# Optimization experiments

Measured on AMD Instinct MI355X. Metric: run time of the kernel, lower is better.

The kernel has to match this reference:

```python
import jax, jax.numpy as jnp
import numpy as np

B, T, D_OBS = 64, 512, 128
D_LAT, D_HID, K = 16, 256, 8
VAR = 0.0005
LOG2PI = float(np.log(2.0 * np.pi))


def _leaky(x):
    return jnp.where(x > 0, x, 0.01 * x)


def setup_inputs() -> dict:
    key = jax.random.key(0)
    ks = jax.random.split(key, 12)
    s = 0.05
    return {
        "x": jax.random.normal(ks[0], (B, T, D_OBS), jnp.float32),
        "eps": jax.random.normal(ks[1], (B, T, D_LAT), jnp.float32),
        "W1": jax.random.normal(ks[2], (D_OBS, D_HID), jnp.float32) * s,
        "b1": jnp.zeros((D_HID,), jnp.float32),
        "W2": jax.random.normal(ks[3], (D_HID, 2 * D_LAT), jnp.float32) * s,
        "b2": jnp.zeros((2 * D_LAT,), jnp.float32),
        "Wt1": jax.random.normal(ks[4], (K, D_LAT, D_HID), jnp.float32) * s,
        "bt1": jnp.zeros((K, D_HID), jnp.float32),
        "Wt2": jax.random.normal(ks[5], (K, D_HID, D_LAT), jnp.float32) * s,
        "bt2": jnp.zeros((K, D_LAT), jnp.float32),
        "Wd1": jax.random.normal(ks[6], (D_LAT, D_HID), jnp.float32) * s,
        "bd1": jnp.zeros((D_HID,), jnp.float32),
        "Wd2": jax.random.normal(ks[7], (D_HID, D_OBS), jnp.float32) * s,
        "bd2": jnp.zeros((D_OBS,), jnp.float32),
        "Q": jax.random.normal(ks[8], (K, K), jnp.float32) * 0.1,
        "pi": jax.random.normal(ks[9], (K,), jnp.float32) * 0.1,
        "init_mean": jax.random.normal(ks[10], (K, D_LAT), jnp.float32),
        "init_cov": jax.random.uniform(ks[11], (K, 1, 1), jnp.float32) * jnp.eye(D_LAT, dtype=jnp.float32)[None] * 5.0,
        "covs": jnp.tile(jnp.eye(D_LAT, dtype=jnp.float32)[None], (K, 1, 1)),
    }


def _mvn_logprob(diff, chol):
    # diff [..., K, d]; chol [K, d, d] lower Cholesky of per-state covariance
    d = chol.shape[-1]
    Linv = jax.scipy.linalg.solve_triangular(
        chol, jnp.broadcast_to(jnp.eye(d, dtype=chol.dtype), chol.shape), lower=True)
    sol = jnp.einsum('kij,...kj->...ki', Linv, diff)
    logdet = 2.0 * jnp.sum(jnp.log(jnp.diagonal(chol, axis1=-2, axis2=-1)), -1)  # [K]
    return -0.5 * (d * LOG2PI + logdet + jnp.sum(sol * sol, -1))


def _forward(x, eps, W1, b1, W2, b2, Wt1, bt1, Wt2, bt2, Wd1, bd1, Wd2, bd2,
             Q, pi, init_mean, init_cov, covs):
    Bx = x.shape[0]
    dz = init_mean.shape[-1]
    # ---- factored MLP encoder: x -> (mu, logvar); reparameterized sample ----
    h = _leaky(x @ W1 + b1)
    enc = h @ W2 + b2
    z_mu, z_log_var = enc[..., :dz], enc[..., dz:]
    z = z_mu + jnp.exp(0.5 * z_log_var) * eps                            # [B,T,dz]
    # ---- local evidence log p(z_t | z_{t-1}, s_t=k) ----
    jitter = 1e-6 * jnp.eye(dz, dtype=x.dtype)
    L0 = jnp.linalg.cholesky(init_cov @ jnp.swapaxes(init_cov, -1, -2) + jitter)
    ev1 = _mvn_logprob(z[:, 0:1, None, :] - init_mean[None, None], L0)   # [B,1,K]
    ht = jax.nn.softplus(jnp.einsum('btd,kdh->btkh', z[:, :-1], Wt1) + bt1)
    means = jnp.einsum('btkh,khd->btkd', ht, Wt2) + bt2                  # [B,T-1,K,dz]
    Lt = jnp.linalg.cholesky(covs @ jnp.swapaxes(covs, -1, -2) + jitter)
    evT = _mvn_logprob(z[:, 1:, None, :] - means, Lt)                    # [B,T-1,K]
    ev = jnp.concatenate([ev1, evT], axis=1)                             # [B,T,K]
    # ---- HMM alpha recursion in log domain (temperature=1) ----
    log_pi = jax.nn.log_softmax(pi)
    Qlog = jax.nn.log_softmax(Q, axis=-1).T                              # [new, old]
    lp0 = ev[:, 0] + log_pi
    lZ0 = jax.scipy.special.logsumexp(lp0, axis=-1)
    la0 = lp0 - lZ0[:, None]

    def step(la, ev_t):
        lp = jax.scipy.special.logsumexp(ev_t[:, :, None] + Qlog[None] + la[:, None, :], axis=-1)
        lZ = jax.scipy.special.logsumexp(lp, axis=-1)
        return lp - lZ[:, None], lZ

    _, lZs = jax.lax.scan(step, la0, jnp.moveaxis(ev[:, 1:], 1, 0))
    log_Z = lZ0 + jnp.sum(lZs, axis=0)                                   # [B]
    # ---- decoder ----
    x_hat = _leaky(z @ Wd1 + bd1) @ Wd2 + bd2
    # ---- ELBO ----
    recon = jnp.sum(-0.5 * jnp.log(2.0 * jnp.pi * VAR) - (x - x_hat) ** 2 / (2.0 * VAR)) / Bx
    logq = -0.5 * (dz * LOG2PI + jnp.sum(z_log_var, -1)
                   + jnp.sum((z - z_mu) ** 2 / jnp.exp(z_log_var), -1))
    entropy_q = -jnp.sum(logq) / Bx
    msm = jnp.sum(log_Z) / Bx
    loss = -(recon + entropy_q + msm)
    return x_hat, z, loss


def reference(x, eps, W1, b1, W2, b2, Wt1, bt1, Wt2, bt2, Wd1, bd1, Wd2, bd2,
              Q, pi, init_mean, init_cov, covs):
    return _forward(x, eps, W1, b1, W2, b2, Wt1, bt1, Wt2, bt2, Wd1, bd1, Wd2, bd2,
                    Q, pi, init_mean, init_cov, covs)
```

## Files before the change

### kernel.cpp

```cpp
#include <hip/hip_runtime.h>
#include <math.h>

#define B_SZ   64
#define T_SZ   512
#define DOBS   128
#define DLAT   16
#define DHID   256
#define K_SZ   8
#define ROWS_T 32704
#define ROWS_A 32768

#define LOG2PI_F 1.8378770664093453f
#define VAR_F    5.0e-4f

#define LINV0_OFF   16
#define LOGDET0_OFF 2064
#define LINVT_OFF   2080
#define LOGDETT_OFF 4128

#define Z_OUT_OFF   4194304
#define LOSS_OFF    4718592
#define PBUF_OFF  262144
#define ACC_OFF   327680

typedef __attribute__((ext_vector_type(8))) short short8;
typedef __attribute__((ext_vector_type(4))) float floatx4;

__device__ __forceinline__ float leakyf(float v) { return v > 0.f ? v : 0.01f * v; }
__device__ __forceinline__ unsigned short f2bf(float f) {
  union { float f; unsigned int u; } v; v.f = f;
  unsigned int lsb = (v.u >> 16) & 1;
  v.u += 0x7fffu + lsb;
  return (unsigned short)(v.u >> 16);
}

__global__ __launch_bounds__(256) void prep_kernel(const float* __restrict__ init_cov,
                                                   const float* __restrict__ covs,
                                                   float* __restrict__ ws) {
  __shared__ float M[16][16];
  __shared__ float L[16][16];
  __shared__ float X[16][17];
  int job = blockIdx.x;
  const float* C = (job < 8) ? (init_cov + job * 256) : (covs + (job - 8) * 256);
  float* linv = ws + ((job < 8) ? (LINV0_OFF + job * 256) : (LINVT_OFF + (job - 8) * 256));
  float* logdet = ws + ((job < 8) ? (LOGDET0_OFF + job) : (LOGDETT_OFF + (job - 8)));
  int tid = threadIdx.x;
  int i = tid >> 4, j = tid & 15;
  {
    float s = (i == j) ? 1e-6f : 0.f;
    #pragma unroll
    for (int p = 0; p < 16; ++p) s += C[i * 16 + p] * C[j * 16 + p];
    M[i][j] = s;
  }
  __syncthreads();
  for (int c = 0; c < 16; ++c) {
    if (tid == 0) {
      float s = M[c][c];
      for (int p = 0; p < c; ++p) s -= L[c][p] * L[c][p];
      L[c][c] = sqrtf(s);
    }
    __syncthreads();
    if (tid > c && tid < 16) {
      float s = M[tid][c];
      for (int p = 0; p < c; ++p) s -= L[tid][p] * L[c][p];
      L[tid][c] = s / L[c][c];
    }
    __syncthreads();
  }
  if (tid < 16) {
    for (int r = 0; r < 16; ++r) {
      float s = (r == tid) ? 1.f : 0.f;
      for (int p = tid; p < r; ++p) s -= L[r][p] * X[p][tid];
      X[r][tid] = (r >= tid) ? s / L[r][r] : 0.f;
    }
  }
  __syncthreads();
  linv[i * 16 + j] = X[i][j];
  if (tid == 0) {
    float s = 0.f;
    for (int d = 0; d < 16; ++d) s += logf(L[d][d]);
    *logdet = 2.f * s;
  }
}

__global__ __launch_bounds__(256) void enc_kernel(
    const float* __restrict__ x, const float* __restrict__ eps,
    const float* __restrict__ W1, const float* __restrict__ b1,
    const float* __restrict__ W2, const float* __restrict__ b2,
    float* __restrict__ z_out, float* __restrict__ ws) {
  __shared__ __align__(16) unsigned short w1t[256 * 136];
  __shared__ __align__(16) unsigned short w2t[32 * 264];
  __shared__ __align__(16) unsigned short hbuf[4 * 16 * 264];
  __shared__ float sred;
  int tid = threadIdx.x;
  if (tid == 0) sred = 0.f;
  for (int e = tid; e < 32768; e += 256) {
    int k = e >> 8, n = e & 255;
    w1t[n * 136 + k] = f2bf(W1[e]);
  }
  for (int e = tid; e < 8192; e += 256) {
    int k = e >> 5, n = e & 31;
    w2t[n * 264 + k] = f2bf(W2[e]);
  }
  __syncthreads();

  int wid = tid >> 6, lane = tid & 63;
  int m = lane & 15, quad = lane >> 4;
  unsigned short* hb = hbuf + wid * (16 * 264);
  float logq_acc = 0.f;

  #pragma unroll
  for (int tile = 0; tile < 2; ++tile) {
    long rowb = (long)blockIdx.x * 128 + wid * 32 + tile * 16;
    short8 xa[4];
    const float* xp = x + (rowb + m) * 128 + quad * 8;
    #pragma unroll
    for (int kt = 0; kt < 4; ++kt) {
      float4 f0 = *(const float4*)(xp + kt * 32);
      float4 f1 = *(const float4*)(xp + kt * 32 + 4);
      short8 v;
      v[0] = (short)f2bf(f0.x); v[1] = (short)f2bf(f0.y);
      v[2] = (short)f2bf(f0.z); v[3] = (short)f2bf(f0.w);
      v[4] = (short)f2bf(f1.x); v[5] = (short)f2bf(f1.y);
      v[6] = (short)f2bf(f1.z); v[7] = (short)f2bf(f1.w);
      xa[kt] = v;
    }
    #pragma unroll 4
    for (int c = 0; c < 16; ++c) {
      float bias = b1[c * 16 + m];
      floatx4 a1 = {bias, bias, bias, bias};
      #pragma unroll
      for (int kt = 0; kt < 4; ++kt) {
        short8 bf = *(const short8*)&w1t[(c * 16 + m) * 136 + kt * 32 + quad * 8];
        a1 = __builtin_amdgcn_mfma_f32_16x16x32_bf16(xa[kt], bf, a1, 0, 0, 0);
      }
      #pragma unroll
      for (int g = 0; g < 4; ++g)
        hb[(quad * 4 + g) * 264 + c * 16 + m] = f2bf(leakyf(a1[g]));
    }
    float bm0 = b2[m], bm1 = b2[16 + m];
    floatx4 a20 = {bm0, bm0, bm0, bm0};
    floatx4 a21 = {bm1, bm1, bm1, bm1};
    #pragma unroll
    for (int kt = 0; kt < 8; ++kt) {
      short8 ha = *(const short8*)&hb[m * 264 + kt * 32 + quad * 8];
      short8 wb0 = *(const short8*)&w2t[m * 264 + kt * 32 + quad * 8];
      short8 wb1 = *(const short8*)&w2t[(16 + m) * 264 + kt * 32 + quad * 8];
      a20 = __builtin_amdgcn_mfma_f32_16x16x32_bf16(ha, wb0, a20, 0, 0, 0);
      a21 = __builtin_amdgcn_mfma_f32_16x16x32_bf16(ha, wb1, a21, 0, 0, 0);
    }
    #pragma unroll
    for (int g = 0; g < 4; ++g) {
      long row = rowb + quad * 4 + g;
      float mu = a20[g], lv = a21[g];
      float ev = eps[row * 16 + m];
      float zv = mu + __expf(0.5f * lv) * ev;
      z_out[row * 16 + m] = zv;
      float zz = zv - mu;
      logq_acc += lv + zz * zz * __expf(-lv);
    }
  }
  #pragma unroll
  for (int off = 1; off < 64; off <<= 1) logq_acc += __shfl_xor(logq_acc, off, 64);
  if (lane == 0) atomicAdd(&sred, -0.5f * logq_acc);
  __syncthreads();
  if (tid == 0) atomicAdd(&ws[1], sred - 0.5f * 16.f * LOG2PI_F * 128.f);
}

__global__ __launch_bounds__(256) void ev0_kernel(const float* __restrict__ z,
                                                  const float* __restrict__ init_mean,
                                                  const float* __restrict__ ws,
                                                  float* __restrict__ evT) {
  int gid = blockIdx.x * 256 + threadIdx.x;
  if (gid >= B_SZ * K_SZ) return;
  int k = gid & 7, b = gid >> 3;
  const float* zr = z + (long)b * T_SZ * 16;
  const float* linv = ws + LINV0_OFF + k * 256;
  float diff[16];
  #pragma unroll
  for (int d = 0; d < 16; ++d) diff[d] = zr[d] - init_mean[k * 16 + d];
  float quad = 0.f;
  #pragma unroll
  for (int i2 = 0; i2 < 16; ++i2) {
    float s = 0.f;
    #pragma unroll
    for (int jj = 0; jj < 16; ++jj) s += linv[i2 * 16 + jj] * diff[jj];
    quad += s * s;
  }
  evT[(long)b * 4096 + (long)k * 512] =
      -0.5f * (16.f * LOG2PI_F + ws[LOGDET0_OFF + k] + quad);
}

__global__ __launch_bounds__(256) void evt_kernel(
    const float* __restrict__ z, const float* __restrict__ Wt1,
    const float* __restrict__ bt1, const float* __restrict__ Wt2,
    const float* __restrict__ bt2, const float* __restrict__ ws,
    float* __restrict__ evT) {
  __shared__ __align__(16) unsigned short w1t[256 * 24];
  __shared__ __align__(16) unsigned short w2t[16 * 264];
  __shared__ __align__(16) unsigned short hbuf[4 * 16 * 264];
  __shared__ __align__(16) unsigned short dbuf[4 * 16 * 24];
  __shared__ __align__(16) unsigned short linvb[16 * 24];
  int tid = threadIdx.x;
  int k = blockIdx.y;
  const float* w1g = Wt1 + k * 4096;
  const float* w2g = Wt2 + k * 4096;
  #pragma unroll
  for (int it = 0; it < 16; ++it)
    w1t[tid * 24 + it] = f2bf(w1g[it * 256 + tid]);
  #pragma unroll
  for (int it = 0; it < 16; ++it) {
    int e = tid + it * 256;
    w2t[(e & 15) * 264 + (e >> 4)] = f2bf(w2g[e]);
  }
  { int i = tid >> 4, j = tid & 15;
    linvb[i * 24 + j] = f2bf(ws[LINVT_OFF + k * 256 + tid]); }
  float logdetk = ws[LOGDETT_OFF + k];
  __syncthreads();

  int wid = tid >> 6;
  int lane = tid & 63;
  int m = lane & 15, quad = lane >> 4;
  long wave_base = (long)blockIdx.x * 64 + wid * 16;
  unsigned short* hb = hbuf + wid * (16 * 264);
  unsigned short* db = dbuf + wid * (16 * 24);

  short8 za = (short8)0;
  if (quad < 2) {
    const float* zp = z + (wave_base + m) * 16 + quad * 8;
    float4 f0 = *(const float4*)zp;
    float4 f1 = *(const float4*)(zp + 4);
    za[0] = (short)f2bf(f0.x); za[1] = (short)f2bf(f0.y);
    za[2] = (short)f2bf(f0.z); za[3] = (short)f2bf(f0.w);
    za[4] = (short)f2bf(f1.x); za[5] = (short)f2bf(f1.y);
    za[6] = (short)f2bf(f1.z); za[7] = (short)f2bf(f1.w);
  }

  const float* bt1g = bt1 + k * 256;
  #pragma unroll 4
  for (int c = 0; c < 16; ++c) {
    short8 bfrag = (short8)0;
    if (quad < 2) bfrag = *(const short8*)&w1t[(c * 16 + m) * 24 + quad * 8];
    float bias = bt1g[c * 16 + m];
    floatx4 a1 = {bias, bias, bias, bias};
    a1 = __builtin_amdgcn_mfma_f32_16x16x32_bf16(za, bfrag, a1, 0, 0, 0);
    #pragma unroll
    for (int g = 0; g < 4; ++g) {
      float v = a1[g];
      float t = __expf(-fabsf(v));
      float sp = fmaxf(v, 0.f) + __logf(1.f + t);
      hb[(quad * 4 + g) * 264 + c * 16 + m] = f2bf(sp);
    }
  }

  float btv = bt2[k * 16 + m];
  floatx4 a2 = {btv, btv, btv, btv};
  #pragma unroll
  for (int kt = 0; kt < 8; ++kt) {
    short8 ha = *(const short8*)&hb[m * 264 + kt * 32 + quad * 8];
    short8 wb = *(const short8*)&w2t[m * 264 + kt * 32 + quad * 8];
    a2 = __builtin_amdgcn_mfma_f32_16x16x32_bf16(ha, wb, a2, 0, 0, 0);
  }

  #pragma unroll
  for (int g = 0; g < 4; ++g) {
    long grow = wave_base + quad * 4 + g;
    float znx = (grow + 1 < ROWS_A) ? z[(grow + 1) * 16 + m] : 0.f;
    db[(quad * 4 + g) * 24 + m] = f2bf(znx - a2[g]);
  }
  short8 da = (short8)0, lb = (short8)0;
  if (quad < 2) {
    da = *(const short8*)&db[m * 24 + quad * 8];
    lb = *(const short8*)&linvb[m * 24 + quad * 8];
  }
  floatx4 a3 = {0.f, 0.f, 0.f, 0.f};
  a3 = __builtin_amdgcn_mfma_f32_16x16x32_bf16(da, lb, a3, 0, 0, 0);
  #pragma unroll
  for (int g = 0; g < 4; ++g) {
    float v = a3[g];
    v = v * v;
    v += __shfl_xor(v, 1, 64);
    v += __shfl_xor(v, 2, 64);
    v += __shfl_xor(v, 4, 64);
    v += __shfl_xor(v, 8, 64);
    long grow = wave_base + quad * 4 + g;
    if (m == 0 && (grow & 511) != 511) {
      long r1 = grow + 1;
      evT[(r1 >> 9) * 4096 + (long)k * 512 + (r1 & 511)] =
          -0.5f * (16.f * LOG2PI_F + logdetk + v);
    }
  }
}

__global__ __launch_bounds__(256) void hmm_scan(const float* __restrict__ Q,
                                                const float* __restrict__ evT,
                                                float* __restrict__ pbuf,
                                                float* __restrict__ accbuf) {
  int tid = threadIdx.x;
  int wid = tid >> 6, lane = tid & 63;
  int job = blockIdx.x * 4 + wid;
  int b = job >> 4, c = job & 15;
  int i = lane >> 3, j = lane & 7;

  float qp[8];
  #pragma unroll
  for (int p = 0; p < 8; ++p) {
    float mr = Q[p * 8 + 0];
    #pragma unroll
    for (int cc = 1; cc < 8; ++cc) mr = fmaxf(mr, Q[p * 8 + cc]);
    float rs = 0.f;
    #pragma unroll
    for (int cc = 0; cc < 8; ++cc) rs += __expf(Q[p * 8 + cc] - mr);
    qp[p] = __expf(Q[p * 8 + i] - mr) / rs;
  }
  float qself;
  {
    float mr = Q[j * 8 + 0];
    #pragma unroll
    for (int cc = 1; cc < 8; ++cc) mr = fmaxf(mr, Q[j * 8 + cc]);
    float rs = 0.f;
    #pragma unroll
    for (int cc = 0; cc < 8; ++cc) rs += __expf(Q[j * 8 + cc] - mr);
    qself = __expf(Q[j * 8 + i] - mr) / rs;
  }

  int t0 = 1 + c * 32;
  int L = (c == 15) ? 31 : 32;
  const float* evI = evT + (long)b * 4096 + (long)i * 512 + t0;

  float f[32];
  float accm = 0.f;
  #pragma unroll
  for (int s = 0; s < 32; ++s) {
    float e = (s < L) ? evI[s] : 0.f;
    float m = e;
    m = fmaxf(m, __shfl_xor(m, 8, 64));
    m = fmaxf(m, __shfl_xor(m, 16, 64));
    m = fmaxf(m, __shfl_xor(m, 32, 64));
    f[s] = __expf(e - m);
    if (s < L) accm += m;
  }

  float P = f[0] * qself;
  #pragma unroll
  for (int s = 1; s < 32; ++s) {
    if (s < L) {
      float a0 = __shfl(P, j,      64);
      float a1 = __shfl(P, 8 + j,  64);
      float a2 = __shfl(P, 16 + j, 64);
      float a3 = __shfl(P, 24 + j, 64);
      float a4 = __shfl(P, 32 + j, 64);
      float a5 = __shfl(P, 40 + j, 64);
      float a6 = __shfl(P, 48 + j, 64);
      float a7 = __shfl(P, 56 + j, 64);
      float sv = ((qp[0] * a0 + qp[1] * a1) + (qp[2] * a2 + qp[3] * a3))
               + ((qp[4] * a4 + qp[5] * a5) + (qp[6] * a6 + qp[7] * a7));
      P = f[s] * sv;
    }
    if ((s & 7) == 7) {
      float mx = P;
      mx = fmaxf(mx, __shfl_xor(mx, 1, 64));
      mx = fmaxf(mx, __shfl_xor(mx, 2, 64));
      mx = fmaxf(mx, __shfl_xor(mx, 4, 64));
      mx = fmaxf(mx, __shfl_xor(mx, 8, 64));
      mx = fmaxf(mx, __shfl_xor(mx, 16, 64));
      mx = fmaxf(mx, __shfl_xor(mx, 32, 64));
      mx = fmaxf(mx, 1e-30f);
      P = P / mx;
      accm += __logf(mx);
    }
  }
  pbuf[(long)job * 64 + lane] = P;
  if (lane == 0) accbuf[job] = accm;
}

__global__ __launch_bounds__(512) void hmm_comb(const float* __restrict__ pi,
                                                const float* __restrict__ evT,
                                                const float* __restrict__ pbuf,
                                                const float* __restrict__ accbuf,
                                                float* __restrict__ ws) {
  int tid = threadIdx.x;
  int wid = tid >> 6, lane = tid & 63;
  int b = blockIdx.x * 8 + wid;
  int j = lane & 7;

  float mp = pi[0];
  #pragma unroll
  for (int cc = 1; cc < 8; ++cc) mp = fmaxf(mp, pi[cc]);
  float sp = 0.f;
  #pragma unroll
  for (int cc = 0; cc < 8; ++cc) sp += __expf(pi[cc] - mp);
  float lpi = pi[j] - mp - __logf(sp);

  float lp0 = evT[(long)b * 4096 + (long)j * 512] + lpi;
  float m0 = lp0;
  m0 = fmaxf(m0, __shfl_xor(m0, 1, 64));
  m0 = fmaxf(m0, __shfl_xor(m0, 2, 64));
  m0 = fmaxf(m0, __shfl_xor(m0, 4, 64));
  float u = __expf(lp0 - m0);
  double acc = (double)m0;

  #pragma unroll
  for (int c = 0; c < 16; ++c) {
    float P = pbuf[((long)b * 16 + c) * 64 + lane];
    float contrib = P * u;
    contrib += __shfl_xor(contrib, 1, 64);
    contrib += __shfl_xor(contrib, 2, 64);
    contrib += __shfl_xor(contrib, 4, 64);
    u = __shfl(contrib, j * 9, 64);
    float mxu = u;
    mxu = fmaxf(mxu, __shfl_xor(mxu, 1, 64));
    mxu = fmaxf(mxu, __shfl_xor(mxu, 2, 64));
    mxu = fmaxf(mxu, __shfl_xor(mxu, 4, 64));
    mxu = fmaxf(mxu, 1e-30f);
    u = u / mxu;
    acc += (double)(__logf(mxu) + accbuf[b * 16 + c]);
  }
  float su = u;
  su += __shfl_xor(su, 1, 64);
  su += __shfl_xor(su, 2, 64);
  su += __shfl_xor(su, 4, 64);
  float logZ = (float)(acc + (double)__logf(su));
  if (lane == 0) atomicAdd(&ws[2], logZ);
}

__global__ __launch_bounds__(256) void dec_kernel(
    const float* __restrict__ x, const float* __restrict__ z,
    const float* __restrict__ Wd1, const float* __restrict__ bd1,
    const float* __restrict__ Wd2, const float* __restrict__ bd2,
    float* __restrict__ xhat, float* __restrict__ ws) {
  __shared__ __align__(16) unsigned short w1t[256 * 24];
  __shared__ __align__(16) unsigned short w2t[128 * 264];
  __shared__ __align__(16) unsigned short hbuf[4 * 16 * 264];
  __shared__ float sred;
  int tid = threadIdx.x;
  if (tid == 0) sred = 0.f;
  for (int e = tid; e < 4096; e += 256) {
    int k = e >> 8, n = e & 255;
    w1t[n * 24 + k] = f2bf(Wd1[e]);
  }
  for (int e = tid; e < 32768; e += 256) {
    int k = e >> 7, n = e & 127;
    w2t[n * 264 + k] = f2bf(Wd2[e]);
  }
  __syncthreads();

  int wid = tid >> 6, lane = tid & 63;
  int m = lane & 15, quad = lane >> 4;
  unsigned short* hb = hbuf + wid * (16 * 264);
  const float C0 = -0.5f * logf(6.2831853071795864f * VAR_F);
  float rsum = 0.f;

  #pragma unroll
  for (int tile = 0; tile < 2; ++tile) {
    long rowb = (long)blockIdx.x * 128 + wid * 32 + tile * 16;
    short8 za = (short8)0;
    if (quad < 2) {
      const float* zp = z + (rowb + m) * 16 + quad * 8;
      float4 f0 = *(const float4*)zp;
      float4 f1 = *(const float4*)(zp + 4);
      za[0] = (short)f2bf(f0.x); za[1] = (short)f2bf(f0.y);
      za[2] = (short)f2bf(f0.z); za[3] = (short)f2bf(f0.w);
      za[4] = (short)f2bf(f1.x); za[5] = (short)f2bf(f1.y);
      za[6] = (short)f2bf(f1.z); za[7] = (short)f2bf(f1.w);
    }
    #pragma unroll 4
    for (int c = 0; c < 16; ++c) {
      short8 bfrag = (short8)0;
      if (quad < 2) bfrag = *(const short8*)&w1t[(c * 16 + m) * 24 + quad * 8];
      float bias = bd1[c * 16 + m];
      floatx4 a1 = {bias, bias, bias, bias};
      a1 = __builtin_amdgcn_mfma_f32_16x16x32_bf16(za, bfrag, a1, 0, 0, 0);
      #pragma unroll
      for (int g = 0; g < 4; ++g)
        hb[(quad * 4 + g) * 264 + c * 16 + m] = f2bf(leakyf(a1[g]));
    }
    floatx4 a2[8];
    #pragma unroll
    for (int c2 = 0; c2 < 8; ++c2) {
      float bv = bd2[c2 * 16 + m];
      a2[c2] = (floatx4){bv, bv, bv, bv};
    }
    #pragma unroll
    for (int kt = 0; kt < 8; ++kt) {
      short8 ha = *(const short8*)&hb[m * 264 + kt * 32 + quad * 8];
      #pragma unroll
      for (int c2 = 0; c2 < 8; ++c2) {
        short8 wb = *(const short8*)&w2t[(c2 * 16 + m) * 264 + kt * 32 + quad * 8];
        a2[c2] = __builtin_amdgcn_mfma_f32_16x16x32_bf16(ha, wb, a2[c2], 0, 0, 0);
      }
    }
    #pragma unroll
    for (int c2 = 0; c2 < 8; ++c2) {
      int col = c2 * 16 + m;
      #pragma unroll
      for (int g = 0; g < 4; ++g) {
        long row = rowb + quad * 4 + g;
        float xh = a2[c2][g];
        xhat[row * 128 + col] = xh;
        float dd = x[row * 128 + col] - xh;
        rsum += C0 - dd * dd * (0.5f / VAR_F);
      }
    }
  }
  #pragma unroll
  for (int off = 1; off < 64; off <<= 1) rsum += __shfl_xor(rsum, off, 64);
  if (lane == 0) atomicAdd(&sred, rsum);
  __syncthreads();
  if (tid == 0) atomicAdd(&ws[0], sred);
}

__global__ void fin_kernel(const float* __restrict__ ws, float* __restrict__ out) {
  float loss = -((ws[0] - ws[1] + ws[2]) * (1.f / 64.f));
  out[LOSS_OFF] = loss;
}

extern "C" void kernel_launch(void* const* d_in, const int* in_sizes, int n_in,
                              void* d_out, int out_size, void* d_ws, size_t ws_size,
                              hipStream_t stream) {
  (void)in_sizes; (void)n_in; (void)out_size; (void)ws_size;
  const float* x   = (const float*)d_in[0];
  const float* eps = (const float*)d_in[1];
  const float* W1  = (const float*)d_in[2];
  const float* b1  = (const float*)d_in[3];
  const float* W2  = (const float*)d_in[4];
  const float* b2  = (const float*)d_in[5];
  const float* Wt1 = (const float*)d_in[6];
  const float* bt1 = (const float*)d_in[7];
  const float* Wt2 = (const float*)d_in[8];
  const float* bt2 = (const float*)d_in[9];
  const float* Wd1 = (const float*)d_in[10];
  const float* bd1 = (const float*)d_in[11];
  const float* Wd2 = (const float*)d_in[12];
  const float* bd2 = (const float*)d_in[13];
  const float* Q   = (const float*)d_in[14];
  const float* pi  = (const float*)d_in[15];
  const float* im  = (const float*)d_in[16];
  const float* ic  = (const float*)d_in[17];
  const float* cv  = (const float*)d_in[18];
  float* out = (float*)d_out;
  float* ws  = (float*)d_ws;
  float* z_out = out + Z_OUT_OFF;
  float* evT  = out;
  float* pbuf = out + PBUF_OFF;
  float* accb = out + ACC_OFF;

  hipMemsetAsync(ws, 0, 16, stream);
  prep_kernel<<<16, 256, 0, stream>>>(ic, cv, ws);
  enc_kernel<<<256, 256, 0, stream>>>(x, eps, W1, b1, W2, b2, z_out, ws);
  ev0_kernel<<<2, 256, 0, stream>>>(z_out, im, ws, evT);
  evt_kernel<<<dim3(512, 8), 256, 0, stream>>>(z_out, Wt1, bt1, Wt2, bt2, ws, evT);
  hmm_scan<<<256, 256, 0, stream>>>(Q, evT, pbuf, accb);
  hmm_comb<<<8, 512, 0, stream>>>(pi, evT, pbuf, accb, ws);
  dec_kernel<<<256, 256, 0, stream>>>(x, z_out, Wd1, bd1, Wd2, bd2, out, ws);
  fin_kernel<<<1, 1, 0, stream>>>(ws, out);
}
```

Measured before the change: 261.9 us.

## Preconvert weights to bf16 image once and restructure enc/evt/dec MLP kernels

Adds a single wcvt kernel that converts and transposes all weights into a padded bf16 image in workspace, so enc/evt/dec no longer re-convert weights per block. Enc and dec now read W1/Wd2 fragments straight from global memory and fuse the hidden-layer chunk into the second GEMM through a small per-wave tile, which cuts LDS use and lets the grid grow to 512 blocks. Evt handles four tiles per block with fewer blocks, folding the first-step emission into hmm_comb and removing ev0_kernel. The memset moves into prep_kernel. The catch is an extra launch plus global-memory weight fragment reads that may cost more than they save.

After: 252.2 us. 1.04x faster.

```diff
diff --git a/kernel.cpp b/kernel.cpp
--- a/kernel.cpp
+++ b/kernel.cpp
@@ -7,7 +7,6 @@
 #define DLAT   16
 #define DHID   256
 #define K_SZ   8
-#define ROWS_T 32704
 #define ROWS_A 32768
 
 #define LOG2PI_F 1.8378770664093453f
@@ -17,6 +16,16 @@
 #define LOGDET0_OFF 2064
 #define LINVT_OFF   2080
 #define LOGDETT_OFF 4128
+#define WIMG_F_OFF  8192
+
+#define EVT_W1   0
+#define EVT_W2   49152
+#define EVT_LINV 82944
+#define ENC_W1   86016
+#define ENC_W2   120832
+#define DEC_W1   129280
+#define DEC_W2   135424
+#define WCVT_TOTAL 141568
 
 #define Z_OUT_OFF   4194304
 #define LOSS_OFF    4718592
@@ -24,6 +33,7 @@
 #define ACC_OFF   327680
 
 typedef __attribute__((ext_vector_type(8))) short short8;
+typedef __attribute__((ext_vector_type(8))) unsigned short ush8;
 typedef __attribute__((ext_vector_type(4))) float floatx4;
 
 __device__ __forceinline__ float leakyf(float v) { return v > 0.f ? v : 0.01f * v; }
@@ -45,6 +55,7 @@
   float* linv = ws + ((job < 8) ? (LINV0_OFF + job * 256) : (LINVT_OFF + (job - 8) * 256));
   float* logdet = ws + ((job < 8) ? (LOGDET0_OFF + job) : (LOGDETT_OFF + (job - 8)));
   int tid = threadIdx.x;
+  if (job == 0 && tid < 4) ws[tid] = 0.f;
   int i = tid >> 4, j = tid & 15;
   {
     float s = (i == j) ? 1e-6f : 0.f;
@@ -83,211 +94,209 @@
   }
 }
 
+__global__ __launch_bounds__(256) void wcvt_kernel(
+    const float* __restrict__ Wt1, const float* __restrict__ Wt2,
+    const float* __restrict__ W1, const float* __restrict__ W2,
+    const float* __restrict__ Wd1, const float* __restrict__ Wd2,
+    const float* __restrict__ ws, unsigned short* __restrict__ wimg) {
+  for (int e = blockIdx.x * 256 + threadIdx.x; e < WCVT_TOTAL; e += gridDim.x * 256) {
+    if (e < 32768) {
+      int k = e >> 12, r = e & 4095, i = r >> 4, d = r & 15;
+      wimg[EVT_W1 + k * 6144 + i * 24 + d] = f2bf(Wt1[k * 4096 + d * 256 + i]);
+    } else if (e < 65536) {
+      int e2 = e - 32768; int k = e2 >> 12, r = e2 & 4095, h = r >> 4, d2 = r & 15;
+      wimg[EVT_W2 + k * 4224 + d2 * 264 + h] = f2bf(Wt2[k * 4096 + h * 16 + d2]);
+    } else if (e < 67584) {
+      int e2 = e - 65536; int k = e2 >> 8, r = e2 & 255, i = r >> 4, j = r & 15;
+      wimg[EVT_LINV + k * 384 + i * 24 + j] = f2bf(ws[LINVT_OFF + k * 256 + i * 16 + j]);
+    } else if (e < 100352) {
+      int e2 = e - 67584; int n = e2 >> 7, kk = e2 & 127;
+      wimg[ENC_W1 + n * 136 + kk] = f2bf(W1[kk * 256 + n]);
+    } else if (e < 108544) {
+      int e2 = e - 100352; int n = e2 >> 8, kk = e2 & 255;
+      wimg[ENC_W2 + n * 264 + kk] = f2bf(W2[kk * 32 + n]);
+    } else if (e < 112640) {
+      int e2 = e - 108544; int n = e2 >> 4, kk = e2 & 15;
+      wimg[DEC_W1 + n * 24 + kk] = f2bf(Wd1[kk * 256 + n]);
+    } else {
+      int e2 = e - 112640; int n = e2 & 127, kk = e2 >> 7;
+      wimg[DEC_W2 + n * 264 + kk] = f2bf(Wd2[kk * 128 + n]);
+    }
+  }
+}
+
 __global__ __launch_bounds__(256) void enc_kernel(
     const float* __restrict__ x, const float* __restrict__ eps,
-    const float* __restrict__ W1, const float* __restrict__ b1,
-    const float* __restrict__ W2, const float* __restrict__ b2,
+    const float* __restrict__ b1, const float* __restrict__ b2,
+    const unsigned short* __restrict__ wimg,
     float* __restrict__ z_out, float* __restrict__ ws) {
-  __shared__ __align__(16) unsigned short w1t[256 * 136];
   __shared__ __align__(16) unsigned short w2t[32 * 264];
-  __shared__ __align__(16) unsigned short hbuf[4 * 16 * 264];
+  __shared__ __align__(16) unsigned short ttile[4][16 * 56];
+  __shared__ float b1s[256];
   __shared__ float sred;
   int tid = threadIdx.x;
   if (tid == 0) sred = 0.f;
-  for (int e = tid; e < 32768; e += 256) {
-    int k = e >> 8, n = e & 255;
-    w1t[n * 136 + k] = f2bf(W1[e]);
-  }
-  for (int e = tid; e < 8192; e += 256) {
-    int k = e >> 5, n = e & 31;
-    w2t[n * 264 + k] = f2bf(W2[e]);
+  {
+    const ush8* s2 = (const ush8*)(wimg + ENC_W2);
+    for (int e = tid; e < 1056; e += 256) ((ush8*)w2t)[e] = s2[e];
+    b1s[tid] = b1[tid];
   }
   __syncthreads();
 
   int wid = tid >> 6, lane = tid & 63;
   int m = lane & 15, quad = lane >> 4;
-  unsigned short* hb = hbuf + wid * (16 * 264);
-  float logq_acc = 0.f;
-
-  #pragma unroll
-  for (int tile = 0; tile < 2; ++tile) {
-    long rowb = (long)blockIdx.x * 128 + wid * 32 + tile * 16;
-    short8 xa[4];
-    const float* xp = x + (rowb + m) * 128 + quad * 8;
-    #pragma unroll
-    for (int kt = 0; kt < 4; ++kt) {
-      float4 f0 = *(const float4*)(xp + kt * 32);
-      float4 f1 = *(const float4*)(xp + kt * 32 + 4);
-      short8 v;
-      v[0] = (short)f2bf(f0.x); v[1] = (short)f2bf(f0.y);
-      v[2] = (short)f2bf(f0.z); v[3] = (short)f2bf(f0.w);
-      v[4] = (short)f2bf(f1.x); v[5] = (short)f2bf(f1.y);
-      v[6] = (short)f2bf(f1.z); v[7] = (short)f2bf(f1.w);
-      xa[kt] = v;
-    }
-    #pragma unroll 4
-    for (int c = 0; c < 16; ++c) {
-      float bias = b1[c * 16 + m];
+  unsigned short* tt = ttile[wid];
+  const unsigned short* w1i = wimg + ENC_W1;
+  long rowb = (long)blockIdx.x * 64 + wid * 16;
+
+  short8 xa[4];
+  const float* xp = x + (rowb + m) * 128 + quad * 8;
+  #pragma unroll
+  for (int kt = 0; kt < 4; ++kt) {
+    float4 f0 = *(const float4*)(xp + kt * 32);
+    float4 f1 = *(const float4*)(xp + kt * 32 + 4);
+    short8 v;
+    v[0] = (short)f2bf(f0.x); v[1] = (short)f2bf(f0.y);
+    v[2] = (short)f2bf(f0.z); v[3] = (short)f2bf(f0.w);
+    v[4] = (short)f2bf(f1.x); v[5] = (short)f2bf(f1.y);
+    v[6] = (short)f2bf(f1.z); v[7] = (short)f2bf(f1.w);
+    xa[kt] = v;
+  }
+  float bm0 = b2[m], bm1 = b2[16 + m];
+  floatx4 a20 = {bm0, bm0, bm0, bm0};
+  floatx4 a21 = {bm1, bm1, bm1, bm1};
+  #pragma unroll
+  for (int cp = 0; cp < 8; ++cp) {
+    #pragma unroll
+    for (int h = 0; h < 2; ++h) {
+      int c = cp * 2 + h;
+      float bias = b1s[c * 16 + m];
       floatx4 a1 = {bias, bias, bias, bias};
       #pragma unroll
       for (int kt = 0; kt < 4; ++kt) {
-        short8 bf = *(const short8*)&w1t[(c * 16 + m) * 136 + kt * 32 + quad * 8];
+        short8 bf = *(const short8*)&w1i[(c * 16 + m) * 136 + kt * 32 + quad * 8];
         a1 = __builtin_amdgcn_mfma_f32_16x16x32_bf16(xa[kt], bf, a1, 0, 0, 0);
       }
       #pragma unroll
       for (int g = 0; g < 4; ++g)
-        hb[(quad * 4 + g) * 264 + c * 16 + m] = f2bf(leakyf(a1[g]));
-    }
-    float bm0 = b2[m], bm1 = b2[16 + m];
-    floatx4 a20 = {bm0, bm0, bm0, bm0};
-    floatx4 a21 = {bm1, bm1, bm1, bm1};
-    #pragma unroll
-    for (int kt = 0; kt < 8; ++kt) {
-      short8 ha = *(const short8*)&hb[m * 264 + kt * 32 + quad * 8];
-      short8 wb0 = *(const short8*)&w2t[m * 264 + kt * 32 + quad * 8];
-      short8 wb1 = *(const short8*)&w2t[(16 + m) * 264 + kt * 32 + quad * 8];
-      a20 = __builtin_amdgcn_mfma_f32_16x16x32_bf16(ha, wb0, a20, 0, 0, 0);
-      a21 = __builtin_amdgcn_mfma_f32_16x16x32_bf16(ha, wb1, a21, 0, 0, 0);
-    }
-    #pragma unroll
-    for (int g = 0; g < 4; ++g) {
-      long row = rowb + quad * 4 + g;
-      float mu = a20[g], lv = a21[g];
-      float ev = eps[row * 16 + m];
-      float zv = mu + __expf(0.5f * lv) * ev;
-      z_out[row * 16 + m] = zv;
-      float zz = zv - mu;
-      logq_acc += lv + zz * zz * __expf(-lv);
-    }
+        tt[(quad * 4 + g) * 56 + h * 16 + m] = f2bf(leakyf(a1[g]));
+    }
+    short8 ha = *(const short8*)&tt[m * 56 + quad * 8];
+    short8 wb0 = *(const short8*)&w2t[m * 264 + cp * 32 + quad * 8];
+    short8 wb1 = *(const short8*)&w2t[(16 + m) * 264 + cp * 32 + quad * 8];
+    a20 = __builtin_amdgcn_mfma_f32_16x16x32_bf16(ha, wb0, a20, 0, 0, 0);
+    a21 = __builtin_amdgcn_mfma_f32_16x16x32_bf16(ha, wb1, a21, 0, 0, 0);
+  }
+  float logq_acc = 0.f;
+  #pragma unroll
+  for (int g = 0; g < 4; ++g) {
+    long row = rowb + quad * 4 + g;
+    float mu = a20[g], lv = a21[g];
+    float ev = eps[row * 16 + m];
+    float zv = mu + __expf(0.5f * lv) * ev;
+    z_out[row * 16 + m] = zv;
+    float zz = zv - mu;
+    logq_acc += lv + zz * zz * __expf(-lv);
   }
   #pragma unroll
   for (int off = 1; off < 64; off <<= 1) logq_acc += __shfl_xor(logq_acc, off, 64);
   if (lane == 0) atomicAdd(&sred, -0.5f * logq_acc);
   __syncthreads();
-  if (tid == 0) atomicAdd(&ws[1], sred - 0.5f * 16.f * LOG2PI_F * 128.f);
-}
-
-__global__ __launch_bounds__(256) void ev0_kernel(const float* __restrict__ z,
-                                                  const float* __restrict__ init_mean,
-                                                  const float* __restrict__ ws,
-                                                  float* __restrict__ evT) {
-  int gid = blockIdx.x * 256 + threadIdx.x;
-  if (gid >= B_SZ * K_SZ) return;
-  int k = gid & 7, b = gid >> 3;
-  const float* zr = z + (long)b * T_SZ * 16;
-  const float* linv = ws + LINV0_OFF + k * 256;
-  float diff[16];
-  #pragma unroll
-  for (int d = 0; d < 16; ++d) diff[d] = zr[d] - init_mean[k * 16 + d];
-  float quad = 0.f;
-  #pragma unroll
-  for (int i2 = 0; i2 < 16; ++i2) {
-    float s = 0.f;
-    #pragma unroll
-    for (int jj = 0; jj < 16; ++jj) s += linv[i2 * 16 + jj] * diff[jj];
-    quad += s * s;
-  }
-  evT[(long)b * 4096 + (long)k * 512] =
-      -0.5f * (16.f * LOG2PI_F + ws[LOGDET0_OFF + k] + quad);
+  if (tid == 0) atomicAdd(&ws[1], sred - 0.5f * 16.f * LOG2PI_F * 64.f);
 }
 
 __global__ __launch_bounds__(256) void evt_kernel(
-    const float* __restrict__ z, const float* __restrict__ Wt1,
-    const float* __restrict__ bt1, const float* __restrict__ Wt2,
-    const float* __restrict__ bt2, const float* __restrict__ ws,
-    float* __restrict__ evT) {
-  __shared__ __align__(16) unsigned short w1t[256 * 24];
-  __shared__ __align__(16) unsigned short w2t[16 * 264];
-  __shared__ __align__(16) unsigned short hbuf[4 * 16 * 264];
-  __shared__ __align__(16) unsigned short dbuf[4 * 16 * 24];
-  __shared__ __align__(16) unsigned short linvb[16 * 24];
+    const float* __restrict__ z, const unsigned short* __restrict__ wimg,
+    const float* __restrict__ bt1, const float* __restrict__ bt2,
+    const float* __restrict__ ws, float* __restrict__ evT) {
+  __shared__ __align__(16) unsigned short w1t[6144];
+  __shared__ __align__(16) unsigned short w2t[4224];
+  __shared__ __align__(16) unsigned short linvb[384];
+  __shared__ __align__(16) unsigned short ttile[4][16 * 56];
+  __shared__ __align__(16) unsigned short dtile[4][16 * 24];
+  __shared__ float bt1s[256];
   int tid = threadIdx.x;
   int k = blockIdx.y;
-  const float* w1g = Wt1 + k * 4096;
-  const float* w2g = Wt2 + k * 4096;
-  #pragma unroll
-  for (int it = 0; it < 16; ++it)
-    w1t[tid * 24 + it] = f2bf(w1g[it * 256 + tid]);
-  #pragma unroll
-  for (int it = 0; it < 16; ++it) {
-    int e = tid + it * 256;
-    w2t[(e & 15) * 264 + (e >> 4)] = f2bf(w2g[e]);
-  }
-  { int i = tid >> 4, j = tid & 15;
-    linvb[i * 24 + j] = f2bf(ws[LINVT_OFF + k * 256 + tid]); }
+  {
+    const ush8* s1 = (const ush8*)(wimg + EVT_W1 + k * 6144);
+    for (int e = tid; e < 768; e += 256) ((ush8*)w1t)[e] = s1[e];
+    const ush8* s2 = (const ush8*)(wimg + EVT_W2 + k * 4224);
+    for (int e = tid; e < 528; e += 256) ((ush8*)w2t)[e] = s2[e];
+    if (tid < 48) ((ush8*)linvb)[tid] = ((const ush8*)(wimg + EVT_LINV + k * 384))[tid];
+    bt1s[tid] = bt1[k * 256 + tid];
+  }
   float logdetk = ws[LOGDETT_OFF + k];
   __syncthreads();
 
-  int wid = tid >> 6;
-  int lane = tid & 63;
+  int wid = tid >> 6, lane = tid & 63;
   int m = lane & 15, quad = lane >> 4;
-  long wave_base = (long)blockIdx.x * 64 + wid * 16;
-  unsigned short* hb = hbuf + wid * (16 * 264);
-  unsigned short* db = dbuf + wid * (16 * 24);
-
-  short8 za = (short8)0;
-  if (quad < 2) {
-    const float* zp = z + (wave_base + m) * 16 + quad * 8;
-    float4 f0 = *(const float4*)zp;
-    float4 f1 = *(const float4*)(zp + 4);
-    za[0] = (short)f2bf(f0.x); za[1] = (short)f2bf(f0.y);
-    za[2] = (short)f2bf(f0.z); za[3] = (short)f2bf(f0.w);
-    za[4] = (short)f2bf(f1.x); za[5] = (short)f2bf(f1.y);
-    za[6] = (short)f2bf(f1.z); za[7] = (short)f2bf(f1.w);
-  }
-
-  const float* bt1g = bt1 + k * 256;
-  #pragma unroll 4
-  for (int c = 0; c < 16; ++c) {
-    short8 bfrag = (short8)0;
-    if (quad < 2) bfrag = *(const short8*)&w1t[(c * 16 + m) * 24 + quad * 8];
-    float bias = bt1g[c * 16 + m];
-    floatx4 a1 = {bias, bias, bias, bias};
-    a1 = __builtin_amdgcn_mfma_f32_16x16x32_bf16(za, bfrag, a1, 0, 0, 0);
+  unsigned short* tt = ttile[wid];
+  unsigned short* db = dtile[wid];
+  float btv = bt2[k * 16 + m];
+
+  #pragma unroll
+  for (int tile = 0; tile < 4; ++tile) {
+    long rowb = (long)blockIdx.x * 256 + wid * 64 + tile * 16;
+    short8 za = (short8)0;
+    if (quad < 2) {
+      const float* zp = z + (rowb + m) * 16 + quad * 8;
+      float4 f0 = *(const float4*)zp;
+      float4 f1 = *(const float4*)(zp + 4);
+      za[0] = (short)f2bf(f0.x); za[1] = (short)f2bf(f0.y);
+      za[2] = (short)f2bf(f0.z); za[3] = (short)f2bf(f0.w);
+      za[4] = (short)f2bf(f1.x); za[5] = (short)f2bf(f1.y);
+      za[6] = (short)f2bf(f1.z); za[7] = (short)f2bf(f1.w);
+    }
+    floatx4 a2 = {btv, btv, btv, btv};
+    #pragma unroll
+    for (int cp = 0; cp < 8; ++cp) {
+      #pragma unroll
+      for (int h = 0; h < 2; ++h) {
+        int c = cp * 2 + h;
+        short8 bfrag = (short8)0;
+        if (quad < 2) bfrag = *(const short8*)&w1t[(c * 16 + m) * 24 + quad * 8];
+        float bias = bt1s[c * 16 + m];
+        floatx4 a1 = {bias, bias, bias, bias};
+        a1 = __builtin_amdgcn_mfma_f32_16x16x32_bf16(za, bfrag, a1, 0, 0, 0);
+        #pragma unroll
+        for (int g = 0; g < 4; ++g) {
+          float v = a1[g];
+          float t = __expf(-fabsf(v));
+          float sp = fmaxf(v, 0.f) + __logf(1.f + t);
+          tt[(quad * 4 + g) * 56 + h * 16 + m] = f2bf(sp);
+        }
+      }
+      short8 ha = *(const short8*)&tt[m * 56 + quad * 8];
+      short8 wb = *(const short8*)&w2t[m * 264 + cp * 32 + quad * 8];
+      a2 = __builtin_amdgcn_mfma_f32_16x16x32_bf16(ha, wb, a2, 0, 0, 0);
+    }
     #pragma unroll
     for (int g = 0; g < 4; ++g) {
-      float v = a1[g];
-      float t = __expf(-fabsf(v));
-      float sp = fmaxf(v, 0.f) + __logf(1.f + t);
-      hb[(quad * 4 + g) * 264 + c * 16 + m] = f2bf(sp);
-    }
-  }
-
-  float btv = bt2[k * 16 + m];
-  floatx4 a2 = {btv, btv, btv, btv};
-  #pragma unroll
-  for (int kt = 0; kt < 8; ++kt) {
-    short8 ha = *(const short8*)&hb[m * 264 + kt * 32 + quad * 8];
-    short8 wb = *(const short8*)&w2t[m * 264 + kt * 32 + quad * 8];
-    a2 = __builtin_amdgcn_mfma_f32_16x16x32_bf16(ha, wb, a2, 0, 0, 0);
-  }
-
-  #pragma unroll
-  for (int g = 0; g < 4; ++g) {
-    long grow = wave_base + quad * 4 + g;
-    float znx = (grow + 1 < ROWS_A) ? z[(grow + 1) * 16 + m] : 0.f;
-    db[(quad * 4 + g) * 24 + m] = f2bf(znx - a2[g]);
-  }
-  short8 da = (short8)0, lb = (short8)0;
-  if (quad < 2) {
-    da = *(const short8*)&db[m * 24 + quad * 8];
-    lb = *(const short8*)&linvb[m * 24 + quad * 8];
-  }
-  floatx4 a3 = {0.f, 0.f, 0.f, 0.f};
-  a3 = __builtin_amdgcn_mfma_f32_16x16x32_bf16(da, lb, a3, 0, 0, 0);
-  #pragma unroll
-  for (int g = 0; g < 4; ++g) {
-    float v = a3[g];
-    v = v * v;
-    v += __shfl_xor(v, 1, 64);
-    v += __shfl_xor(v, 2, 64);
-    v += __shfl_xor(v, 4, 64);
-    v += __shfl_xor(v, 8, 64);
-    long grow = wave_base + quad * 4 + g;
-    if (m == 0 && (grow & 511) != 511) {
-      long r1 = grow + 1;
-      evT[(r1 >> 9) * 4096 + (long)k * 512 + (r1 & 511)] =
-          -0.5f * (16.f * LOG2PI_F + logdetk + v);
+      long grow = rowb + quad * 4 + g;
+      float znx = (grow + 1 < ROWS_A) ? z[(grow + 1) * 16 + m] : 0.f;
+      db[(quad * 4 + g) * 24 + m] = f2bf(znx - a2[g]);
+    }
+    short8 da = (short8)0, lb = (short8)0;
+    if (quad < 2) {
+      da = *(const short8*)&db[m * 24 + quad * 8];
+      lb = *(const short8*)&linvb[m * 24 + quad * 8];
+    }
+    floatx4 a3 = {0.f, 0.f, 0.f, 0.f};
+    a3 = __builtin_amdgcn_mfma_f32_16x16x32_bf16(da, lb, a3, 0, 0, 0);
+    #pragma unroll
+    for (int g = 0; g < 4; ++g) {
+      float v = a3[g];
+      v = v * v;
+      v += __shfl_xor(v, 1, 64);
+      v += __shfl_xor(v, 2, 64);
+      v += __shfl_xor(v, 4, 64);
+      v += __shfl_xor(v, 8, 64);
+      long grow = rowb + quad * 4 + g;
+      if (m == 0 && (grow & 511) != 511) {
+        long r1 = grow + 1;
+        evT[(r1 >> 9) * 4096 + (long)k * 512 + (r1 & 511)] =
+            -0.5f * (16.f * LOG2PI_F + logdetk + v);
+      }
     }
   }
 }
@@ -375,7 +384,8 @@
 }
 
 __global__ __launch_bounds__(512) void hmm_comb(const float* __restrict__ pi,
-                                                const float* __restrict__ evT,
+                                                const float* __restrict__ z,
+                                                const float* __restrict__ init_mean,
                                                 const float* __restrict__ pbuf,
                                                 const float* __restrict__ accbuf,
                                                 float* __restrict__ ws) {
@@ -392,7 +402,22 @@
   for (int cc = 0; cc < 8; ++cc) sp += __expf(pi[cc] - mp);
   float lpi = pi[j] - mp - __logf(sp);
 
-  float lp0 = evT[(long)b * 4096 + (long)j * 512] + lpi;
+  const float* zr = z + (long)b * 8192;
+  const float* linv = ws + LINV0_OFF + j * 256;
+  float diff[16];
+  #pragma unroll
+  for (int d = 0; d < 16; ++d) diff[d] = zr[d] - init_mean[j * 16 + d];
+  float quad0 = 0.f;
+  #pragma unroll
+  for (int i2 = 0; i2 < 16; ++i2) {
+    float s = 0.f;
+    #pragma unroll
+    for (int jj = 0; jj < 16; ++jj) s += linv[i2 * 16 + jj] * diff[jj];
+    quad0 += s * s;
+  }
+  float ev0 = -0.5f * (16.f * LOG2PI_F + ws[LOGDET0_OFF + j] + quad0);
+
+  float lp0 = ev0 + lpi;
   float m0 = lp0;
   m0 = fmaxf(m0, __shfl_xor(m0, 1, 64));
   m0 = fmaxf(m0, __shfl_xor(m0, 2, 64));
@@ -426,81 +451,79 @@
 
 __global__ __launch_bounds__(256) void dec_kernel(
     const float* __restrict__ x, const float* __restrict__ z,
-    const float* __restrict__ Wd1, const float* __restrict__ bd1,
-    const float* __restrict__ Wd2, const float* __restrict__ bd2,
+    const float* __restrict__ bd1, const float* __restrict__ bd2,
+    const unsigned short* __restrict__ wimg,
     float* __restrict__ xhat, float* __restrict__ ws) {
-  __shared__ __align__(16) unsigned short w1t[256 * 24];
-  __shared__ __align__(16) unsigned short w2t[128 * 264];
-  __shared__ __align__(16) unsigned short hbuf[4 * 16 * 264];
+  __shared__ __align__(16) unsigned short w1t[6144];
+  __shared__ __align__(16) unsigned short ttile[4][16 * 56];
+  __shared__ float bd1s[256];
+  __shared__ float bd2s[128];
   __shared__ float sred;
   int tid = threadIdx.x;
   if (tid == 0) sred = 0.f;
-  for (int e = tid; e < 4096; e += 256) {
-    int k = e >> 8, n = e & 255;
-    w1t[n * 24 + k] = f2bf(Wd1[e]);
-  }
-  for (int e = tid; e < 32768; e += 256) {
-    int k = e >> 7, n = e & 127;
-    w2t[n * 264 + k] = f2bf(Wd2[e]);
+  {
+    const ush8* s1 = (const ush8*)(wimg + DEC_W1);
+    for (int e = tid; e < 768; e += 256) ((ush8*)w1t)[e] = s1[e];
+    bd1s[tid] = bd1[tid];
+    if (tid < 128) bd2s[tid] = bd2[tid];
   }
   __syncthreads();
 
   int wid = tid >> 6, lane = tid & 63;
   int m = lane & 15, quad = lane >> 4;
-  unsigned short* hb = hbuf + wid * (16 * 264);
-  const float C0 = -0.5f * logf(6.2831853071795864f * VAR_F);
-  float rsum = 0.f;
-
-  #pragma unroll
-  for (int tile = 0; tile < 2; ++tile) {
-    long rowb = (long)blockIdx.x * 128 + wid * 32 + tile * 16;
-    short8 za = (short8)0;
-    if (quad < 2) {
-      const float* zp = z + (rowb + m) * 16 + quad * 8;
-      float4 f0 = *(const float4*)zp;
-      float4 f1 = *(const float4*)(zp + 4);
-      za[0] = (short)f2bf(f0.x); za[1] = (short)f2bf(f0.y);
-      za[2] = (short)f2bf(f0.z); za[3] = (short)f2bf(f0.w);
-      za[4] = (short)f2bf(f1.x); za[5] = (short)f2bf(f1.y);
-      za[6] = (short)f2bf(f1.z); za[7] = (short)f2bf(f1.w);
-    }
-    #pragma unroll 4
-    for (int c = 0; c < 16; ++c) {
+  unsigned short* tt = ttile[wid];
+  const unsigned short* w2i = wimg + DEC_W2;
+  long rowb = (long)blockIdx.x * 64 + wid * 16;
+
+  short8 za = (short8)0;
+  if (quad < 2) {
+    const float* zp = z + (rowb + m) * 16 + quad * 8;
+    float4 f0 = *(const float4*)zp;
+    float4 f1 = *(const float4*)(zp + 4);
+    za[0] = (short)f2bf(f0.x); za[1] = (short)f2bf(f0.y);
+    za[2] = (short)f2bf(f0.z); za[3] = (short)f2bf(f0.w);
+    za[4] = (short)f2bf(f1.x); za[5] = (short)f2bf(f1.y);
+    za[6] = (short)f2bf(f1.z); za[7] = (short)f2bf(f1.w);
+  }
+  floatx4 a2[8];
+  #pragma unroll
+  for (int c2 = 0; c2 < 8; ++c2) {
+    float bv = bd2s[c2 * 16 + m];
+    a2[c2] = (floatx4){bv, bv, bv, bv};
+  }
+  #pragma unroll
+  for (int cp = 0; cp < 8; ++cp) {
+    #pragma unroll
+    for (int h = 0; h < 2; ++h) {
+      int c = cp * 2 + h;
       short8 bfrag = (short8)0;
       if (quad < 2) bfrag = *(const short8*)&w1t[(c * 16 + m) * 24 + quad * 8];
-      float bias = bd1[c * 16 + m];
+      float bias = bd1s[c * 16 + m];
       floatx4 a1 = {bias, bias, bias, bias};
       a1 = __builtin_amdgcn_mfma_f32_16x16x32_bf16(za, bfrag, a1, 0, 0, 0);
       #pragma unroll
       for (int g = 0; g < 4; ++g)
-        hb[(quad * 4 + g) * 264 + c * 16 + m] = f2bf(leakyf(a1[g]));
-    }
-    floatx4 a2[8];
+        tt[(quad * 4 + g) * 56 + h * 16 + m] = f2bf(leakyf(a1[g]));
+    }
+    short8 ha = *(const short8*)&tt[m * 56 + quad * 8];
     #pragma unroll
     for (int c2 = 0; c2 < 8; ++c2) {
-      float bv = bd2[c2 * 16 + m];
-      a2[c2] = (floatx4){bv, bv, bv, bv};
-    }
-    #pragma unroll
-    for (int kt = 0; kt < 8; ++kt) {
-      short8 ha = *(const short8*)&hb[m * 264 + kt * 32 + quad * 8];
-      #pragma unroll
-      for (int c2 = 0; c2 < 8; ++c2) {
-        short8 wb = *(const short8*)&w2t[(c2 * 16 + m) * 264 + kt * 32 + quad * 8];
-        a2[c2] = __builtin_amdgcn_mfma_f32_16x16x32_bf16(ha, wb, a2[c2], 0, 0, 0);
-      }
-    }
-    #pragma unroll
-    for (int c2 = 0; c2 < 8; ++c2) {
-      int col = c2 * 16 + m;
-      #pragma unroll
-      for (int g = 0; g < 4; ++g) {
-        long row = rowb + quad * 4 + g;
-        float xh = a2[c2][g];
-        xhat[row * 128 + col] = xh;
-        float dd = x[row * 128 + col] - xh;
-        rsum += C0 - dd * dd * (0.5f / VAR_F);
-      }
+      short8 wb = *(const short8*)&w2i[(c2 * 16 + m) * 264 + cp * 32 + quad * 8];
+      a2[c2] = __builtin_amdgcn_mfma_f32_16x16x32_bf16(ha, wb, a2[c2], 0, 0, 0);
+    }
+  }
+  const float C0 = -0.5f * logf(6.2831853071795864f * VAR_F);
+  float rsum = 0.f;
+  #pragma unroll
+  for (int c2 = 0; c2 < 8; ++c2) {
+    int col = c2 * 16 + m;
+    #pragma unroll
+    for (int g = 0; g < 4; ++g) {
+      long row = rowb + quad * 4 + g;
+      float xh = a2[c2][g];
+      xhat[row * 128 + col] = xh;
+      float dd = x[row * 128 + col] - xh;
+      rsum += C0 - dd * dd * (0.5f / VAR_F);
     }
   }
   #pragma unroll
@@ -544,14 +567,14 @@
   float* evT  = out;
   float* pbuf = out + PBUF_OFF;
   float* accb = out + ACC_OFF;
-
-  hipMemsetAsync(ws, 0, 16, stream);
+  unsigned short* wimg = (unsigned short*)(ws + WIMG_F_OFF);
+
   prep_kernel<<<16, 256, 0, stream>>>(ic, cv, ws);
-  enc_kernel<<<256, 256, 0, stream>>>(x, eps, W1, b1, W2, b2, z_out, ws);
-  ev0_kernel<<<2, 256, 0, stream>>>(z_out, im, ws, evT);
-  evt_kernel<<<dim3(512, 8), 256, 0, stream>>>(z_out, Wt1, bt1, Wt2, bt2, ws, evT);
+  wcvt_kernel<<<144, 256, 0, stream>>>(Wt1, Wt2, W1, W2, Wd1, Wd2, ws, wimg);
+  enc_kernel<<<512, 256, 0, stream>>>(x, eps, b1, b2, wimg, z_out, ws);
+  evt_kernel<<<dim3(128, 8), 256, 0, stream>>>(z_out, wimg, bt1, bt2, ws, evT);
   hmm_scan<<<256, 256, 0, stream>>>(Q, evT, pbuf, accb);
-  hmm_comb<<<8, 512, 0, stream>>>(pi, evT, pbuf, accb, ws);
-  dec_kernel<<<256, 256, 0, stream>>>(x, z_out, Wd1, bd1, Wd2, bd2, out, ws);
+  hmm_comb<<<8, 512, 0, stream>>>(pi, z_out, im, pbuf, accb, ws);
+  dec_kernel<<<512, 256, 0, stream>>>(x, z_out, bd1, bd2, wimg, out, ws);
   fin_kernel<<<1, 1, 0, stream>>>(ws, out);
 }
```
